# Kernel optimization log

Hardware: AMD Instinct MI355X
Metric: run time of the kernel (lower is better)

The kernel has to match this reference:

```python
import jax, jax.numpy as jnp
import numpy as np

B, S, D, H = 2, 2048, 768, 12
DH = D // H


def setup_inputs() -> dict:
    key = jax.random.key(0)
    ks = jax.random.split(key, 12)
    f32 = jnp.float32
    sd = 1.0 / np.sqrt(D)
    return {
        "q": jax.random.normal(ks[0], (B, S, D), f32),
        "k": jax.random.normal(ks[1], (B, S, D), f32),
        "v": jax.random.normal(ks[2], (B, S, D), f32),
        "mask": jax.random.normal(ks[3], (S, S), f32),
        "Wq": jax.random.normal(ks[4], (D, D), f32) * sd,
        "bq": jnp.zeros((D,), f32),
        "Wk": jax.random.normal(ks[5], (D, D), f32) * sd,
        "bk": jnp.zeros((D,), f32),
        "Wv": jax.random.normal(ks[6], (D, D), f32) * sd,
        "bv": jnp.zeros((D,), f32),
        "Wo": jax.random.normal(ks[7], (D, D), f32) * sd,
        "bo": jnp.zeros((D,), f32),
    }


def reference(q, k, v, mask, Wq, bq, Wk, bk, Wv, bv, Wo, bo):
    # torch nn.Linear: y = x @ W.T + b
    qh = (q @ Wq.T + bq).reshape(B, S, H, DH).transpose(0, 2, 1, 3)  # [B,H,S,DH]
    kh = (k @ Wk.T + bk).reshape(B, S, H, DH).transpose(0, 2, 1, 3)
    vh = (v @ Wv.T + bv).reshape(B, S, H, DH).transpose(0, 2, 1, 3)
    scores = jnp.einsum("bhsd,bhtd->bhst", qh, kh)  # [B,H,S,S]
    # original adds mask after permute to [H,B,S,S]; with an [S,S] mask the
    # broadcast add is identical either way
    scores = scores + mask
    attn = jax.nn.softmax(scores.astype(jnp.float32) / np.sqrt(DH), axis=-1)
    out = jnp.einsum("bhst,bhtd->bhsd", attn, vh)  # [B,H,S,DH]
    out = out.transpose(0, 2, 1, 3).reshape(B, S, D)
    return out @ Wo.T + bo
```

## Files before the change

### kernel.cpp

```cpp
#include <hip/hip_runtime.h>
#include <hip/hip_bf16.h>

#define B_ 2
#define S_ 2048
#define D_ 768
#define H_ 12
#define DH_ 64
#define M_ (B_*S_)
#define BH_ (B_*H_)

typedef __bf16 v8bf __attribute__((ext_vector_type(8)));
typedef __bf16 v4bf __attribute__((ext_vector_type(4)));
typedef float  v4f  __attribute__((ext_vector_type(4)));

static __device__ __forceinline__ v4f mfma16(v8bf a, v8bf b, v4f c) {
  return __builtin_amdgcn_mfma_f32_16x16x32_bf16(a, b, c, 0, 0, 0);
}

static __device__ __forceinline__ void gload_lds16(const __bf16* g, __bf16* l) {
  __builtin_amdgcn_global_load_lds(
      (const __attribute__((address_space(1))) unsigned int*)g,
      (__attribute__((address_space(3))) unsigned int*)l,
      16, 0, 0);
}

#define C1_ 0.18033688011112042f

__global__ __launch_bounds__(256) void convert_kernel(
    const float* __restrict__ q, const float* __restrict__ k, const float* __restrict__ v,
    const float* __restrict__ Wq, const float* __restrict__ Wk,
    const float* __restrict__ Wv, const float* __restrict__ Wo,
    __bf16* __restrict__ Xq, __bf16* __restrict__ Xk, __bf16* __restrict__ Xv,
    __bf16* __restrict__ Wqb, __bf16* __restrict__ Wkb,
    __bf16* __restrict__ Wvb, __bf16* __restrict__ Wob)
{
  const float* src; __bf16* dst; int n;
  switch (blockIdx.y) {
    case 0: src = q;  dst = Xq;  n = M_*D_; break;
    case 1: src = k;  dst = Xk;  n = M_*D_; break;
    case 2: src = v;  dst = Xv;  n = M_*D_; break;
    case 3: src = Wq; dst = Wqb; n = D_*D_; break;
    case 4: src = Wk; dst = Wkb; n = D_*D_; break;
    case 5: src = Wv; dst = Wvb; n = D_*D_; break;
    default: src = Wo; dst = Wob; n = D_*D_; break;
  }
  int n4 = n >> 2;
  for (int i = blockIdx.x*blockDim.x + threadIdx.x; i < n4; i += gridDim.x*blockDim.x) {
    float4 x = ((const float4*)src)[i];
    v4bf y;
    y[0] = (__bf16)x.x; y[1] = (__bf16)x.y; y[2] = (__bf16)x.z; y[3] = (__bf16)x.w;
    ((v4bf*)dst)[i] = y;
  }
}

__global__ __launch_bounds__(256) void em_kernel(
    const float* __restrict__ mask, __bf16* __restrict__ em)
{
  int t = blockIdx.x*256 + threadIdx.x;
  int L = t & 63; int rest = t >> 6;
  int qq = rest & 3; rest >>= 2;
  int ktile = rest & 63; rest >>= 6;
  int qt = rest;
  int row = qt*64 + qq*16 + (L & 15);
  int key0 = ktile*32 + ((L >> 4) << 2);
  const float* mp = mask + (size_t)row*S_ + key0;
  float4 m0 = *(const float4*)mp;
  float4 m1 = *(const float4*)(mp + 16);
  v8bf e;
  e[0] = (__bf16)exp2f(C1_*m0.x); e[1] = (__bf16)exp2f(C1_*m0.y);
  e[2] = (__bf16)exp2f(C1_*m0.z); e[3] = (__bf16)exp2f(C1_*m0.w);
  e[4] = (__bf16)exp2f(C1_*m1.x); e[5] = (__bf16)exp2f(C1_*m1.y);
  e[6] = (__bf16)exp2f(C1_*m1.z); e[7] = (__bf16)exp2f(C1_*m1.w);
  *(v8bf*)(em + (size_t)t*8) = e;
}

template<int BM, int BN>
static __device__ __forceinline__ void gemm_core_lds(
    const __bf16* __restrict__ A, const __bf16* __restrict__ W,
    int m0, int n0, __bf16* lds, v4f acc[BM/32][BN/32])
{
  constexpr int NFA = BM/16, NFB = BN/16;
  constexpr int PW  = (NFA + NFB) / 4;
  constexpr int MI  = BM/32, NJ = BN/32;
  const int lane = threadIdx.x & 63;
  const int wave = threadIdx.x >> 6;
  const int r16 = lane & 15;
  const int kc8 = (lane >> 4) << 3;
  const int ia = (wave >> 1) * MI;
  const int ib = (wave & 1) * NJ;

  const __bf16* gsrc[PW]; __bf16* ldst[PW];
  #pragma unroll
  for (int t = 0; t < PW; t++) {
    int fb = wave*PW + t;
    gsrc[t] = (fb < NFA)
        ? A + (size_t)(m0 + fb*16 + r16)*D_ + kc8
        : W + (size_t)(n0 + (fb - NFA)*16 + r16)*D_ + kc8;
    ldst[t] = lds + fb*512;
  }

  for (int k0 = 0; k0 < D_; k0 += 32) {
    #pragma unroll
    for (int t = 0; t < PW; t++) gload_lds16(gsrc[t] + k0, ldst[t]);
    __syncthreads();
    v8bf a[MI], b[NJ];
    #pragma unroll
    for (int i = 0; i < MI; i++) a[i] = *(const v8bf*)(lds + (ia+i)*512 + lane*8);
    #pragma unroll
    for (int j = 0; j < NJ; j++) b[j] = *(const v8bf*)(lds + (NFA+ib+j)*512 + lane*8);
    #pragma unroll
    for (int i = 0; i < MI; i++)
      #pragma unroll
      for (int j = 0; j < NJ; j++)
        acc[i][j] = mfma16(a[i], b[j], acc[i][j]);
    __syncthreads();
  }
}

__global__ __launch_bounds__(256) void qkv_gemm(
    const __bf16* __restrict__ Xq, const __bf16* __restrict__ Xk, const __bf16* __restrict__ Xv,
    const __bf16* __restrict__ Wqb, const __bf16* __restrict__ Wkb, const __bf16* __restrict__ Wvb,
    const float* __restrict__ bq, const float* __restrict__ bk, const float* __restrict__ bv,
    __bf16* __restrict__ qf, __bf16* __restrict__ kf, __bf16* __restrict__ vf)
{
  __shared__ __bf16 lds[(128+64)*32];
  const int mode = blockIdx.z;
  const __bf16* A = (mode == 0) ? Xq : (mode == 1) ? Xk : Xv;
  const __bf16* W = (mode == 0) ? Wqb : (mode == 1) ? Wkb : Wvb;
  const float* bias = (mode == 0) ? bq : (mode == 1) ? bk : bv;
  const int m0 = blockIdx.y << 7, n0 = blockIdx.x << 6;
  v4f acc[4][2];
  #pragma unroll
  for (int i = 0; i < 4; i++)
    #pragma unroll
    for (int j = 0; j < 2; j++) { v4f z = {0.f,0.f,0.f,0.f}; acc[i][j] = z; }
  gemm_core_lds<128,64>(A, W, m0, n0, lds, acc);

  const int lane = threadIdx.x & 63;
  const int wave = threadIdx.x >> 6;
  const int wm = (wave >> 1) << 6, wn = (wave & 1) << 5;
  const int col = lane & 15, quad = lane >> 4;
  float bb[2]; int nn[2];
  #pragma unroll
  for (int j = 0; j < 2; j++) { nn[j] = n0 + wn + 16*j + col; bb[j] = bias[nn[j]]; }

  if (mode < 2) {
    __bf16* dst = (mode == 0) ? qf : kf;
    const float sc = (mode == 0) ? C1_ : 1.0f;
    #pragma unroll
    for (int i = 0; i < 4; i++)
      #pragma unroll
      for (int r = 0; r < 4; r++) {
        int m = m0 + wm + 16*i + quad*4 + r;
        int batch = m >> 11, s = m & (S_-1);
        #pragma unroll
        for (int j = 0; j < 2; j++) {
          int n = nn[j];
          int h = n >> 6, dd = n & 63;
          size_t flat = (((size_t)(batch*H_ + h)*128 + (s >> 4))*2 + (dd >> 5))*512
                      + ((((dd >> 3) & 3)*16 + (s & 15)) << 3) + (dd & 7);
          dst[flat] = (__bf16)((acc[i][j][r] + bb[j]) * sc);
        }
      }
  } else {
    #pragma unroll
    for (int i = 0; i < 4; i++) {
      int mbase = m0 + wm + 16*i + quad*4;
      int batch = mbase >> 11, s0 = mbase & (S_-1);
      #pragma unroll
      for (int j = 0; j < 2; j++) {
        int n = nn[j];
        int h = n >> 6, dd = n & 63;
        v4bf pk;
        #pragma unroll
        for (int r = 0; r < 4; r++) pk[r] = (__bf16)(acc[i][j][r] + bb[j]);
        size_t flat = (((size_t)(batch*H_ + h)*64 + (s0 >> 5))*4 + (dd >> 4))*512
                    + ((((s0 >> 3) & 3)*16 + (dd & 15)) << 3) + (s0 & 7);
        *(v4bf*)(vf + flat) = pk;
      }
    }
  }
}

__global__ __launch_bounds__(256, 3) void attn_kernel(
    const __bf16* __restrict__ qf, const __bf16* __restrict__ kf, const __bf16* __restrict__ vf,
    const __bf16* __restrict__ em, __bf16* __restrict__ ao)
{
  __shared__ __bf16 plds[4][4][16][40];
  __shared__ float ls[4][64];
  __shared__ float Ored[64][68];

  const int bh = blockIdx.y;
  const int wave = threadIdx.x >> 6, lane = threadIdx.x & 63;
  const int col = lane & 15, quad = lane >> 4, koff = quad << 3;
  const int q0 = blockIdx.x << 6;
  const int batch = bh / H_, h = bh % H_;
  const __bf16* qfb = qf + (size_t)bh * (S_*DH_);
  const __bf16* kfb = kf + (size_t)bh * (S_*DH_);
  const __bf16* vfb = vf + (size_t)bh * (S_*DH_);
  const __bf16* emb = em + (size_t)(q0 >> 6) * 131072;
  __bf16 (*pt)[16][40] = plds[wave];

  v8bf Qf[4][2];
  #pragma unroll
  for (int qq = 0; qq < 4; qq++) {
    const __bf16* qblk = qfb + (size_t)((q0 >> 4) + qq)*1024;
    Qf[qq][0] = *(const v8bf*)(qblk + lane*8);
    Qf[qq][1] = *(const v8bf*)(qblk + 512 + lane*8);
  }

  v4f O[4][4];
  #pragma unroll
  for (int f = 0; f < 4; f++)
    #pragma unroll
    for (int qq = 0; qq < 4; qq++) { v4f z = {0.f,0.f,0.f,0.f}; O[f][qq] = z; }
  float li[4];
  #pragma unroll
  for (int qq = 0; qq < 4; qq++) li[qq] = 0.f;

  const int kbeg = wave << 9;

  const __bf16* kblk0 = kfb + (size_t)(kbeg >> 4)*1024;
  v8bf Ka0 = *(const v8bf*)(kblk0 + lane*8);
  v8bf Ka1 = *(const v8bf*)(kblk0 + 512 + lane*8);
  v8bf Ka2 = *(const v8bf*)(kblk0 + 1024 + lane*8);
  v8bf Ka3 = *(const v8bf*)(kblk0 + 1536 + lane*8);

  #pragma unroll 1
  for (int kt = kbeg; kt < kbeg + 512; kt += 32) {
    const __bf16* vblk = vfb + (size_t)(kt >> 5)*2048;
    v8bf Vf0 = *(const v8bf*)(vblk + lane*8);
    v8bf Vf1 = *(const v8bf*)(vblk + 512 + lane*8);
    v8bf Vf2 = *(const v8bf*)(vblk + 1024 + lane*8);
    v8bf Vf3 = *(const v8bf*)(vblk + 1536 + lane*8);
    const __bf16* eblk = emb + (size_t)(kt >> 5)*2048;

    #pragma unroll
    for (int qq = 0; qq < 4; qq++) {
      v8bf ef = *(const v8bf*)(eblk + qq*512 + lane*8);
      v4f s0 = {0.f,0.f,0.f,0.f}, s1 = {0.f,0.f,0.f,0.f};
      s0 = mfma16(Ka0, Qf[qq][0], s0); s0 = mfma16(Ka1, Qf[qq][1], s0);
      s1 = mfma16(Ka2, Qf[qq][0], s1); s1 = mfma16(Ka3, Qf[qq][1], s1);

      float p[8], rs = 0.f;
      #pragma unroll
      for (int j = 0; j < 4; j++) {
        p[j]   = exp2f(s0[j]) * (float)ef[j];
        p[4+j] = exp2f(s1[j]) * (float)ef[4+j];
      }
      #pragma unroll
      for (int j = 0; j < 8; j++) rs += p[j];
      li[qq] += rs;
      v4bf pk0, pk1;
      #pragma unroll
      for (int r = 0; r < 4; r++) { pk0[r] = (__bf16)p[r]; pk1[r] = (__bf16)p[4+r]; }
      *(v4bf*)(&pt[qq][col][quad*4])      = pk0;
      *(v4bf*)(&pt[qq][col][16 + quad*4]) = pk1;
    }

    if (kt + 32 < kbeg + 512) {
      const __bf16* nk = kfb + (size_t)((kt + 32) >> 4)*1024;
      Ka0 = *(const v8bf*)(nk + lane*8);
      Ka1 = *(const v8bf*)(nk + 512 + lane*8);
      Ka2 = *(const v8bf*)(nk + 1024 + lane*8);
      Ka3 = *(const v8bf*)(nk + 1536 + lane*8);
    }

    v8bf Pf[4];
    #pragma unroll
    for (int qq = 0; qq < 4; qq++) Pf[qq] = *(const v8bf*)(&pt[qq][col][koff]);
    #pragma unroll
    for (int qq = 0; qq < 4; qq++) {
      O[0][qq] = mfma16(Vf0, Pf[qq], O[0][qq]);
      O[1][qq] = mfma16(Vf1, Pf[qq], O[1][qq]);
      O[2][qq] = mfma16(Vf2, Pf[qq], O[2][qq]);
      O[3][qq] = mfma16(Vf3, Pf[qq], O[3][qq]);
    }
  }

  #pragma unroll
  for (int qq = 0; qq < 4; qq++) {
    float rs = li[qq];
    rs += __shfl_xor(rs, 16);
    rs += __shfl_xor(rs, 32);
    if (quad == 0) ls[wave][16*qq + col] = rs;
  }
  __syncthreads();

  for (int w = 0; w < 4; w++) {
    if (wave == w) {
      #pragma unroll
      for (int qq = 0; qq < 4; qq++)
        #pragma unroll
        for (int f = 0; f < 4; f++) {
          float4* dst = (float4*)&Ored[16*qq + col][16*f + quad*4];
          float4 val;
          val.x = O[f][qq][0]; val.y = O[f][qq][1];
          val.z = O[f][qq][2]; val.w = O[f][qq][3];
          if (w != 0) {
            float4 old = *dst;
            val.x += old.x; val.y += old.y; val.z += old.z; val.w += old.w;
          }
          *dst = val;
        }
    }
    __syncthreads();
  }
  {
    int q = threadIdx.x >> 2, ds = (threadIdx.x & 3) << 4;
    float lst = ls[0][q] + ls[1][q] + ls[2][q] + ls[3][q];
    float invl = 1.f / lst;
    __bf16* orow = ao + ((size_t)batch*S_ + q0 + q)*D_ + h*DH_ + ds;
    v8bf o0, o1;
    #pragma unroll
    for (int i = 0; i < 8; i++) {
      o0[i] = (__bf16)(Ored[q][ds + i] * invl);
      o1[i] = (__bf16)(Ored[q][ds + 8 + i] * invl);
    }
    *(v8bf*)orow = o0;
    *(v8bf*)(orow + 8) = o1;
  }
}

__global__ __launch_bounds__(256) void out_gemm(
    const __bf16* __restrict__ Ao, const __bf16* __restrict__ Wob,
    const float* __restrict__ bo, float* __restrict__ out)
{
  __shared__ __bf16 lds[(64+64)*32];
  const int m0 = blockIdx.y << 6, n0 = blockIdx.x << 6;
  v4f acc[2][2];
  #pragma unroll
  for (int i = 0; i < 2; i++)
    #pragma unroll
    for (int j = 0; j < 2; j++) { v4f z = {0.f,0.f,0.f,0.f}; acc[i][j] = z; }
  gemm_core_lds<64,64>(Ao, Wob, m0, n0, lds, acc);

  const int lane = threadIdx.x & 63;
  const int wave = threadIdx.x >> 6;
  const int wm = (wave >> 1) << 5, wn = (wave & 1) << 5;
  const int col = lane & 15, quad = lane >> 4;
  float bb[2]; int nn[2];
  #pragma unroll
  for (int j = 0; j < 2; j++) { nn[j] = n0 + wn + 16*j + col; bb[j] = bo[nn[j]]; }
  #pragma unroll
  for (int i = 0; i < 2; i++)
    #pragma unroll
    for (int r = 0; r < 4; r++) {
      int m = m0 + wm + 16*i + quad*4 + r;
      #pragma unroll
      for (int j = 0; j < 2; j++)
        out[(size_t)m*D_ + nn[j]] = acc[i][j][r] + bb[j];
    }
}

extern "C" void kernel_launch(void* const* d_in, const int* in_sizes, int n_in,
                              void* d_out, int out_size, void* d_ws, size_t ws_size,
                              hipStream_t stream)
{
  const float* q    = (const float*)d_in[0];
  const float* k    = (const float*)d_in[1];
  const float* v    = (const float*)d_in[2];
  const float* mask = (const float*)d_in[3];
  const float* Wq   = (const float*)d_in[4];
  const float* bq   = (const float*)d_in[5];
  const float* Wk   = (const float*)d_in[6];
  const float* bk   = (const float*)d_in[7];
  const float* Wv   = (const float*)d_in[8];
  const float* bv   = (const float*)d_in[9];
  const float* Wo   = (const float*)d_in[10];
  const float* bo   = (const float*)d_in[11];

  const size_t XN = (size_t)M_ * D_;
  const size_t WN = (size_t)D_ * D_;
  const size_t HN = (size_t)BH_ * S_ * DH_;

  char* ws = (char*)d_ws;
  __bf16* Xq  = (__bf16*)ws;                 ws += XN * 2;
  __bf16* Xk  = (__bf16*)ws;                 ws += XN * 2;
  __bf16* Xv  = (__bf16*)ws;                 ws += XN * 2;
  __bf16* Wqb = (__bf16*)ws;                 ws += WN * 2;
  __bf16* Wkb = (__bf16*)ws;                 ws += WN * 2;
  __bf16* Wvb = (__bf16*)ws;                 ws += WN * 2;
  __bf16* Wob = (__bf16*)ws;                 ws += WN * 2;
  __bf16* qfb = (__bf16*)ws;                 ws += HN * 2;
  __bf16* kfb = (__bf16*)ws;                 ws += HN * 2;
  __bf16* vfb = (__bf16*)ws;                 ws += HN * 2;
  __bf16* aob = (__bf16*)ws;                 ws += XN * 2;
  __bf16* emb = Xq;

  convert_kernel<<<dim3(3072, 7), 256, 0, stream>>>(
      q, k, v, Wq, Wk, Wv, Wo, Xq, Xk, Xv, Wqb, Wkb, Wvb, Wob);
  qkv_gemm<<<dim3(12, 32, 3), 256, 0, stream>>>(
      Xq, Xk, Xv, Wqb, Wkb, Wvb, bq, bk, bv, qfb, kfb, vfb);
  em_kernel<<<dim3(2048), 256, 0, stream>>>(mask, emb);
  attn_kernel<<<dim3(32, 24), 256, 0, stream>>>(qfb, kfb, vfb, emb, aob);
  out_gemm<<<dim3(12, 64), 256, 0, stream>>>(aob, Wob, bo, (float*)d_out);
}
```

Before: 283.6 us.

## Restructure attention: 128-query blocks with shared double-buffered K/V tiles in LDS

The attention kernel changes from 4 waves that each split the key range, which needed a cross-wave O reduction in LDS, to 8 waves that each own 16 query rows and walk all keys. K and V tiles are loaded once per block into double-buffered LDS with global_load_lds and shared by all waves, which removes per-wave global K/V loads and the final reduction. The exp(mask) layout kernel is re-indexed to match 128-row query tiles. The cost is a block-wide barrier every key tile and fewer independent MFMA chains per wave, which could limit latency hiding.

```diff
diff --git a/kernel.cpp b/kernel.cpp
--- a/kernel.cpp
+++ b/kernel.cpp
@@ -58,11 +58,11 @@
 {
   int t = blockIdx.x*256 + threadIdx.x;
   int L = t & 63; int rest = t >> 6;
-  int qq = rest & 3; rest >>= 2;
-  int ktile = rest & 63; rest >>= 6;
+  int w = rest & 7; rest >>= 3;
+  int kt = rest & 63; rest >>= 6;
   int qt = rest;
-  int row = qt*64 + qq*16 + (L & 15);
-  int key0 = ktile*32 + ((L >> 4) << 2);
+  int row = qt*128 + w*16 + (L & 15);
+  int key0 = kt*32 + ((L >> 4) << 2);
   const float* mp = mask + (size_t)row*S_ + key0;
   float4 m0 = *(const float4*)mp;
   float4 m1 = *(const float4*)(mp + 16);
@@ -182,143 +182,100 @@
   }
 }
 
-__global__ __launch_bounds__(256, 3) void attn_kernel(
+__global__ __launch_bounds__(512, 4) void attn_kernel(
     const __bf16* __restrict__ qf, const __bf16* __restrict__ kf, const __bf16* __restrict__ vf,
     const __bf16* __restrict__ em, __bf16* __restrict__ ao)
 {
-  __shared__ __bf16 plds[4][4][16][40];
-  __shared__ float ls[4][64];
-  __shared__ float Ored[64][68];
+  __shared__ __bf16 kv[2][2][2048];
+  __shared__ __bf16 plds[8][16][40];
 
   const int bh = blockIdx.y;
+  const int qt = blockIdx.x;
   const int wave = threadIdx.x >> 6, lane = threadIdx.x & 63;
   const int col = lane & 15, quad = lane >> 4, koff = quad << 3;
-  const int q0 = blockIdx.x << 6;
   const int batch = bh / H_, h = bh % H_;
   const __bf16* qfb = qf + (size_t)bh * (S_*DH_);
   const __bf16* kfb = kf + (size_t)bh * (S_*DH_);
   const __bf16* vfb = vf + (size_t)bh * (S_*DH_);
-  const __bf16* emb = em + (size_t)(q0 >> 6) * 131072;
-  __bf16 (*pt)[16][40] = plds[wave];
-
-  v8bf Qf[4][2];
-  #pragma unroll
-  for (int qq = 0; qq < 4; qq++) {
-    const __bf16* qblk = qfb + (size_t)((q0 >> 4) + qq)*1024;
-    Qf[qq][0] = *(const v8bf*)(qblk + lane*8);
-    Qf[qq][1] = *(const v8bf*)(qblk + 512 + lane*8);
-  }
-
-  v4f O[4][4];
-  #pragma unroll
-  for (int f = 0; f < 4; f++)
-    #pragma unroll
-    for (int qq = 0; qq < 4; qq++) { v4f z = {0.f,0.f,0.f,0.f}; O[f][qq] = z; }
-  float li[4];
-  #pragma unroll
-  for (int qq = 0; qq < 4; qq++) li[qq] = 0.f;
-
-  const int kbeg = wave << 9;
-
-  const __bf16* kblk0 = kfb + (size_t)(kbeg >> 4)*1024;
-  v8bf Ka0 = *(const v8bf*)(kblk0 + lane*8);
-  v8bf Ka1 = *(const v8bf*)(kblk0 + 512 + lane*8);
-  v8bf Ka2 = *(const v8bf*)(kblk0 + 1024 + lane*8);
-  v8bf Ka3 = *(const v8bf*)(kblk0 + 1536 + lane*8);
-
-  #pragma unroll 1
-  for (int kt = kbeg; kt < kbeg + 512; kt += 32) {
-    const __bf16* vblk = vfb + (size_t)(kt >> 5)*2048;
-    v8bf Vf0 = *(const v8bf*)(vblk + lane*8);
-    v8bf Vf1 = *(const v8bf*)(vblk + 512 + lane*8);
-    v8bf Vf2 = *(const v8bf*)(vblk + 1024 + lane*8);
-    v8bf Vf3 = *(const v8bf*)(vblk + 1536 + lane*8);
-    const __bf16* eblk = emb + (size_t)(kt >> 5)*2048;
-
-    #pragma unroll
-    for (int qq = 0; qq < 4; qq++) {
-      v8bf ef = *(const v8bf*)(eblk + qq*512 + lane*8);
-      v4f s0 = {0.f,0.f,0.f,0.f}, s1 = {0.f,0.f,0.f,0.f};
-      s0 = mfma16(Ka0, Qf[qq][0], s0); s0 = mfma16(Ka1, Qf[qq][1], s0);
-      s1 = mfma16(Ka2, Qf[qq][0], s1); s1 = mfma16(Ka3, Qf[qq][1], s1);
-
-      float p[8], rs = 0.f;
-      #pragma unroll
-      for (int j = 0; j < 4; j++) {
-        p[j]   = exp2f(s0[j]) * (float)ef[j];
-        p[4+j] = exp2f(s1[j]) * (float)ef[4+j];
-      }
-      #pragma unroll
-      for (int j = 0; j < 8; j++) rs += p[j];
-      li[qq] += rs;
-      v4bf pk0, pk1;
-      #pragma unroll
-      for (int r = 0; r < 4; r++) { pk0[r] = (__bf16)p[r]; pk1[r] = (__bf16)p[4+r]; }
-      *(v4bf*)(&pt[qq][col][quad*4])      = pk0;
-      *(v4bf*)(&pt[qq][col][16 + quad*4]) = pk1;
+  const __bf16* emb = em + (size_t)qt * 262144 + wave*512;
+  __bf16 (*pt)[40] = plds[wave];
+
+  const __bf16* qblk = qfb + (size_t)(qt*8 + wave)*1024;
+  v8bf Qf0 = *(const v8bf*)(qblk + lane*8);
+  v8bf Qf1 = *(const v8bf*)(qblk + 512 + lane*8);
+
+  v4f O[4];
+  #pragma unroll
+  for (int f = 0; f < 4; f++) { v4f z = {0.f,0.f,0.f,0.f}; O[f] = z; }
+  float li = 0.f;
+
+  const __bf16* gsrc = ((wave < 4) ? kfb : vfb) + ((wave & 3) << 9) + lane*8;
+  __bf16* ld0 = &kv[0][wave >> 2][(wave & 3) << 9];
+  __bf16* ld1 = &kv[1][wave >> 2][(wave & 3) << 9];
+
+  gload_lds16(gsrc, ld0);
+  __syncthreads();
+
+  #pragma unroll 2
+  for (int kt = 0; kt < 64; kt++) {
+    const int buf = kt & 1;
+    if (kt + 1 < 64)
+      gload_lds16(gsrc + (size_t)(kt + 1)*2048, buf ? ld0 : ld1);
+
+    const __bf16* Kb = kv[buf][0];
+    const __bf16* Vb = kv[buf][1];
+
+    v8bf ef = *(const v8bf*)(emb + kt*4096 + lane*8);
+    v8bf Vf0 = *(const v8bf*)(Vb + lane*8);
+    v8bf Vf1 = *(const v8bf*)(Vb + 512 + lane*8);
+    v8bf Vf2 = *(const v8bf*)(Vb + 1024 + lane*8);
+    v8bf Vf3 = *(const v8bf*)(Vb + 1536 + lane*8);
+    v8bf Ka0 = *(const v8bf*)(Kb + lane*8);
+    v8bf Ka1 = *(const v8bf*)(Kb + 512 + lane*8);
+    v8bf Ka2 = *(const v8bf*)(Kb + 1024 + lane*8);
+    v8bf Ka3 = *(const v8bf*)(Kb + 1536 + lane*8);
+
+    v4f s0 = {0.f,0.f,0.f,0.f}, s1 = {0.f,0.f,0.f,0.f};
+    s0 = mfma16(Ka0, Qf0, s0); s0 = mfma16(Ka1, Qf1, s0);
+    s1 = mfma16(Ka2, Qf0, s1); s1 = mfma16(Ka3, Qf1, s1);
+
+    float p[8], rs = 0.f;
+    #pragma unroll
+    for (int j = 0; j < 4; j++) {
+      p[j]   = exp2f(s0[j]) * (float)ef[j];
+      p[4+j] = exp2f(s1[j]) * (float)ef[4+j];
     }
-
-    if (kt + 32 < kbeg + 512) {
-      const __bf16* nk = kfb + (size_t)((kt + 32) >> 4)*1024;
-      Ka0 = *(const v8bf*)(nk + lane*8);
-      Ka1 = *(const v8bf*)(nk + 512 + lane*8);
-      Ka2 = *(const v8bf*)(nk + 1024 + lane*8);
-      Ka3 = *(const v8bf*)(nk + 1536 + lane*8);
-    }
-
-    v8bf Pf[4];
-    #pragma unroll
-    for (int qq = 0; qq < 4; qq++) Pf[qq] = *(const v8bf*)(&pt[qq][col][koff]);
-    #pragma unroll
-    for (int qq = 0; qq < 4; qq++) {
-      O[0][qq] = mfma16(Vf0, Pf[qq], O[0][qq]);
-      O[1][qq] = mfma16(Vf1, Pf[qq], O[1][qq]);
-      O[2][qq] = mfma16(Vf2, Pf[qq], O[2][qq]);
-      O[3][qq] = mfma16(Vf3, Pf[qq], O[3][qq]);
-    }
-  }
-
-  #pragma unroll
-  for (int qq = 0; qq < 4; qq++) {
-    float rs = li[qq];
-    rs += __shfl_xor(rs, 16);
-    rs += __shfl_xor(rs, 32);
-    if (quad == 0) ls[wave][16*qq + col] = rs;
-  }
-  __syncthreads();
-
-  for (int w = 0; w < 4; w++) {
-    if (wave == w) {
-      #pragma unroll
-      for (int qq = 0; qq < 4; qq++)
-        #pragma unroll
-        for (int f = 0; f < 4; f++) {
-          float4* dst = (float4*)&Ored[16*qq + col][16*f + quad*4];
-          float4 val;
-          val.x = O[f][qq][0]; val.y = O[f][qq][1];
-          val.z = O[f][qq][2]; val.w = O[f][qq][3];
-          if (w != 0) {
-            float4 old = *dst;
-            val.x += old.x; val.y += old.y; val.z += old.z; val.w += old.w;
-          }
-          *dst = val;
-        }
-    }
+    #pragma unroll
+    for (int j = 0; j < 8; j++) rs += p[j];
+    li += rs;
+
+    v4bf pk0, pk1;
+    #pragma unroll
+    for (int r = 0; r < 4; r++) { pk0[r] = (__bf16)p[r]; pk1[r] = (__bf16)p[4+r]; }
+    *(v4bf*)(&pt[col][quad*4])      = pk0;
+    *(v4bf*)(&pt[col][16 + quad*4]) = pk1;
+    v8bf Pf = *(const v8bf*)(&pt[col][koff]);
+
+    O[0] = mfma16(Vf0, Pf, O[0]);
+    O[1] = mfma16(Vf1, Pf, O[1]);
+    O[2] = mfma16(Vf2, Pf, O[2]);
+    O[3] = mfma16(Vf3, Pf, O[3]);
+
     __syncthreads();
   }
-  {
-    int q = threadIdx.x >> 2, ds = (threadIdx.x & 3) << 4;
-    float lst = ls[0][q] + ls[1][q] + ls[2][q] + ls[3][q];
-    float invl = 1.f / lst;
-    __bf16* orow = ao + ((size_t)batch*S_ + q0 + q)*D_ + h*DH_ + ds;
-    v8bf o0, o1;
-    #pragma unroll
-    for (int i = 0; i < 8; i++) {
-      o0[i] = (__bf16)(Ored[q][ds + i] * invl);
-      o1[i] = (__bf16)(Ored[q][ds + 8 + i] * invl);
-    }
-    *(v8bf*)orow = o0;
-    *(v8bf*)(orow + 8) = o1;
+
+  float rs = li;
+  rs += __shfl_xor(rs, 16);
+  rs += __shfl_xor(rs, 32);
+  float invl = 1.f / rs;
+  const int qg = (qt << 7) + (wave << 4) + col;
+  __bf16* orow = ao + ((size_t)batch*S_ + qg)*D_ + h*DH_ + quad*4;
+  #pragma unroll
+  for (int f = 0; f < 4; f++) {
+    v4bf o;
+    #pragma unroll
+    for (int r = 0; r < 4; r++) o[r] = (__bf16)(O[f][r] * invl);
+    *(v4bf*)(orow + f*16) = o;
   }
 }
 
@@ -393,6 +350,6 @@
   qkv_gemm<<<dim3(12, 32, 3), 256, 0, stream>>>(
       Xq, Xk, Xv, Wqb, Wkb, Wvb, bq, bk, bv, qfb, kfb, vfb);
   em_kernel<<<dim3(2048), 256, 0, stream>>>(mask, emb);
-  attn_kernel<<<dim3(32, 24), 256, 0, stream>>>(qfb, kfb, vfb, emb, aob);
+  attn_kernel<<<dim3(16, 24), 512, 0, stream>>>(qfb, kfb, vfb, emb, aob);
   out_gemm<<<dim3(12, 64), 256, 0, stream>>>(aob, Wob, bo, (float*)d_out);
 }
```

New measurement: 259.2 us. -8.6%, faster.
